# Performance work log

Hardware: AMD Instinct MI355X
Metric: run time of the kernel (lower is better)

The kernel has to match this reference:

```python
import jax, jax.numpy as jnp
import numpy as np

N, E, D, H = 50000, 800000, 128, 128


def _uniform_param(key, shape, fan_in):
    bound = 1.0 / np.sqrt(fan_in)
    return jax.random.uniform(key, shape, jnp.float32, -bound, bound)


def setup_inputs() -> dict:
    key = jax.random.key(0)
    ks = jax.random.split(key, 12)
    x = jax.random.normal(ks[0], (N, D), jnp.float32)
    xedge = jax.random.randint(ks[1], (2, E), 0, N, jnp.int64)
    y = jax.random.randint(ks[2], (N,), 0, 2, jnp.int32).astype(bool)
    return {
        "x": x,
        "xedge": xedge,
        "y": y,
        "pretrain": 0,
        # SAGEConv layer 1 (in=D, out=H): lin_l (with bias) applied to mean aggr, lin_r (no bias) to self
        "W1l": _uniform_param(ks[3], (D, H), D),
        "b1l": _uniform_param(ks[4], (H,), D),
        "W1r": _uniform_param(ks[5], (D, H), D),
        # SAGEConv layer 2 (in=H, out=H)
        "W2l": _uniform_param(ks[6], (H, H), H),
        "b2l": _uniform_param(ks[7], (H,), H),
        "W2r": _uniform_param(ks[8], (H, H), H),
        # Decoder weight [H, H]
        "Wdec": _uniform_param(ks[9], (H, H), H),
    }


def sage_conv(h, src, dst, Wl, bl, Wr, num_nodes):
    # gather neighbor features along edges, mean-aggregate by destination
    msgs = h[src]                                            # [E, d]
    agg = jax.ops.segment_sum(msgs, dst, num_segments=num_nodes)
    cnt = jax.ops.segment_sum(jnp.ones((src.shape[0],), h.dtype), dst,
                              num_segments=num_nodes)
    mean = agg / jnp.maximum(cnt, 1.0)[:, None]              # [N, d]
    return mean @ Wl + bl + h @ Wr                           # [N, out]


def reference(x, xedge, y, pretrain, W1l, b1l, W1r, W2l, b2l, W2r, Wdec):
    src, dst = xedge[0], xedge[1]
    n = x.shape[0]
    # Encoder: SAGE = conv1 -> relu -> (dropout: eval identity) -> conv2
    h = jax.nn.relu(sage_conv(x, src, dst, W1l, b1l, W1r, n))
    emb = sage_conv(h, src, dst, W2l, b2l, W2r, n)           # [N, H]
    # Decoder
    dx = emb @ Wdec                                          # [N, H]
    # BCEWithLogits: pos nodes target 1, neg nodes target 0, mean within each group
    ym = y.astype(dx.dtype)                                  # [N]
    n_pos = jnp.sum(ym)
    n_neg = n - n_pos
    hdim = dx.shape[1]
    sp_pos = jax.nn.softplus(-dx)   # bce(logit, 1)
    sp_neg = jax.nn.softplus(dx)    # bce(logit, 0)
    l2 = jnp.sum(sp_pos * ym[:, None]) / (jnp.maximum(n_pos, 1.0) * hdim)
    l1 = jnp.sum(sp_neg * (1.0 - ym)[:, None]) / (jnp.maximum(n_neg, 1.0) * hdim)
    return (l1 + l2, emb)
```

## Files before the change

### kernel.cpp

```cpp
#include <hip/hip_runtime.h>
#include <hip/hip_bf16.h>

#define NDIM 128
#define SCAN_CHUNK 1024

typedef __attribute__((ext_vector_type(8))) short short8;
typedef __attribute__((ext_vector_type(4))) float f32x4;

__device__ __forceinline__ float bf2f(__hip_bfloat16 v) { return __bfloat162float(v); }

__device__ __forceinline__ float ldf(const void* p, long i, int f32) {
    return f32 ? ((const float*)p)[i] : bf2f(((const __hip_bfloat16*)p)[i]);
}
__device__ __forceinline__ void stf(void* p, long i, int f32, float v) {
    if (f32) ((float*)p)[i] = v;
    else     ((__hip_bfloat16*)p)[i] = __float2bfloat16(v);
}
__device__ __forceinline__ short f2bf(float v) {
    __hip_bfloat16 h = __float2bfloat16(v);
    short s;
    __builtin_memcpy(&s, &h, 2);
    return s;
}
__device__ __forceinline__ float bflo(unsigned u) { u <<= 16; float f; __builtin_memcpy(&f, &u, 4); return f; }
__device__ __forceinline__ float bfhi(unsigned u) { u &= 0xffff0000u; float f; __builtin_memcpy(&f, &u, 4); return f; }
__device__ __forceinline__ unsigned packbf(float a, float b) {
    unsigned la = (unsigned short)f2bf(a);
    unsigned hb = (unsigned short)f2bf(b);
    return (hb << 16) | la;
}
__device__ __forceinline__ int aswz(int m, int k) {
    return m * NDIM + ((((k >> 3) ^ (m & 7)) << 3) | (k & 7));
}
__device__ __forceinline__ int wswz(int m, int p) {
    return m * 64 + ((((p >> 2) ^ (m & 7)) << 2) | (p & 3));
}

__global__ void detect_kernel(const int* __restrict__ xedge32,
                              const unsigned int* __restrict__ yw,
                              const unsigned short* __restrict__ xh,
                              int* __restrict__ flags, int* __restrict__ cnt,
                              float* __restrict__ accum, int* __restrict__ npos, int N) {
    const int gid = blockIdx.x * 256 + threadIdx.x;
    for (int i = gid; i < N; i += gridDim.x * 256) cnt[i] = 0;
    if (gid == 0) { accum[0] = 0.f; accum[1] = 0.f; npos[0] = 0; }
    if (blockIdx.x == 0) {
        __shared__ int se, sy, scount;
        const int t = threadIdx.x;
        if (t == 0) { se = 1; sy = 0; scount = 0; }
        __syncthreads();
        for (int i = t; i < 512; i += 256)
            if (xedge32[2 * i + 1] != 0) se = 0;
        for (int i = t; i < 1024; i += 256)
            if (yw[i] > 1u) sy = 1;
        int c = 0;
        for (int i = t; i < 1024; i += 256) {
            int ex = (xh[2 * i] >> 7) & 0xFF;
            if (ex >= 100 && ex <= 150) c++;
        }
        atomicAdd(&scount, c);
        __syncthreads();
        if (t == 0) { flags[0] = se; flags[1] = sy; flags[2] = (scount < 900) ? 1 : 0; }
    }
}


__global__ void prep_kernel(const void* __restrict__ x,
                            const void* __restrict__ W1l, const void* __restrict__ b1l,
                            const void* __restrict__ W1r, const void* __restrict__ W2l,
                            const void* __restrict__ b2l, const void* __restrict__ W2r,
                            const void* __restrict__ Wd, const int* __restrict__ flags,
                            short* __restrict__ T1l, short* __restrict__ T1r,
                            short* __restrict__ T2l, short* __restrict__ T2r,
                            short* __restrict__ Td, float* __restrict__ b1c,
                            float* __restrict__ b2c, unsigned* __restrict__ xb,
                            const int* __restrict__ xedge, int E,
                            int* __restrict__ cnt, int N) {
    const int wf = flags[2];
    const long idx = (long)blockIdx.x * 256 + threadIdx.x;
    if (idx < E) {
        int d = flags[0] ? xedge[2 * (E + idx)] : xedge[E + idx];
        atomicAdd(&cnt[d], 1);
    }
    if (idx < NDIM * NDIM) {
        int k = (int)(idx >> 7), n = (int)(idx & 127);
        int o = n * NDIM + k;
        T1l[o] = f2bf(ldf(W1l, idx, wf));
        T1r[o] = f2bf(ldf(W1r, idx, wf));
        T2l[o] = f2bf(ldf(W2l, idx, wf));
        T2r[o] = f2bf(ldf(W2r, idx, wf));
        Td [o] = f2bf(ldf(Wd , idx, wf));
        if (idx < NDIM) { b1c[idx] = ldf(b1l, idx, wf); b2c[idx] = ldf(b2l, idx, wf); }
    } else {
        long p = idx - NDIM * NDIM;
        long np = (long)N * 64;
        if (p < np) {
            if (wf) {
                float2 v = ((const float2*)x)[p];
                xb[p] = packbf(v.x, v.y);
            } else {
                xb[p] = ((const unsigned*)x)[p];
            }
        }
    }
}


__global__ void scan_partial(const int* __restrict__ cnt, int* __restrict__ bsum, int N) {
    __shared__ int red[256];
    const int t = threadIdx.x;
    const long base = (long)blockIdx.x * SCAN_CHUNK + (long)t * 4;
    int s = 0;
#pragma unroll
    for (int i = 0; i < 4; ++i) { long idx = base + i; if (idx < N) s += cnt[idx]; }
    red[t] = s;
    __syncthreads();
    for (int off = 128; off >= 1; off >>= 1) {
        if (t < off) red[t] += red[t + off];
        __syncthreads();
    }
    if (t == 0) bsum[blockIdx.x] = red[0];
}

__global__ void scan_bsums(const int* __restrict__ bsum, int* __restrict__ boff,
                           int B, int* __restrict__ rowptr, int N) {
    __shared__ int part[1024];
    const int t = threadIdx.x;
    int v = (t < B) ? bsum[t] : 0;
    part[t] = v;
    __syncthreads();
    for (int off = 1; off < 1024; off <<= 1) {
        int u = (t >= off) ? part[t - off] : 0;
        __syncthreads();
        part[t] += u;
        __syncthreads();
    }
    if (t < B) boff[t] = part[t] - v;
    if (t == 1023) rowptr[N] = part[1023];
}

__global__ void scan_scatter(int* __restrict__ cnt, const int* __restrict__ boff,
                             int* __restrict__ rowptr, int N) {
    __shared__ int tsum[256];
    const int t = threadIdx.x;
    const long base = (long)blockIdx.x * SCAN_CHUNK + (long)t * 4;
    int loc[4];
    int s = 0;
#pragma unroll
    for (int i = 0; i < 4; ++i) {
        long idx = base + i;
        int c = (idx < N) ? cnt[idx] : 0;
        loc[i] = s;
        s += c;
    }
    tsum[t] = s;
    __syncthreads();
    for (int off = 1; off < 256; off <<= 1) {
        int u = (t >= off) ? tsum[t - off] : 0;
        __syncthreads();
        tsum[t] += u;
        __syncthreads();
    }
    const int texcl = tsum[t] - s;
    const int b0 = boff[blockIdx.x];
#pragma unroll
    for (int i = 0; i < 4; ++i) {
        long idx = base + i;
        if (idx < N) { rowptr[idx] = b0 + texcl + loc[i]; cnt[idx] = 0; }
    }
}

__global__ void fill_kernel(const int* __restrict__ xedge, int E,
                            const int* __restrict__ flags, const int* __restrict__ rowptr,
                            int* __restrict__ cur, int* __restrict__ col) {
    int e = blockIdx.x * blockDim.x + threadIdx.x;
    if (e >= E) return;
    const int e64 = flags[0];
    int s = e64 ? xedge[2 * e] : xedge[e];
    int d = e64 ? xedge[2 * (E + e)] : xedge[E + e];
    int p = rowptr[d] + atomicAdd(&cur[d], 1);
    col[p] = s;
}


template <bool RELU, int OUTMODE>
__global__ __launch_bounds__(256)
void layer_mfma(const unsigned* __restrict__ Xb, const int* __restrict__ rowptr,
                const int* __restrict__ col, const short* __restrict__ WlT,
                const float* __restrict__ biasc, const short* __restrict__ WrT,
                const int* __restrict__ flags, void* __restrict__ outp,
                unsigned* __restrict__ hemb, int N) {
    __shared__ short AS[2 * 32 * NDIM];
    short* Ms = AS;
    short* Ss = AS + 32 * NDIM;
    unsigned* Msw = (unsigned*)Ms;
    unsigned* Ssw = (unsigned*)Ss;
    const int t = threadIdx.x;
    const int n0 = blockIdx.x * 32;
    const int wf = flags[2];
    {
        const int g = t >> 6, p = t & 63;
        for (int r = g; r < 32; r += 4) {
            int n = n0 + r;
            float m0 = 0.f, m1 = 0.f;
            unsigned su = 0;
            if (n < N) {
                int b = rowptr[n], e = rowptr[n + 1];
                int i = b;
                for (; i + 8 <= e; i += 8) {
                    unsigned u0 = Xb[(long)col[i    ] * 64 + p];
                    unsigned u1 = Xb[(long)col[i + 1] * 64 + p];
                    unsigned u2 = Xb[(long)col[i + 2] * 64 + p];
                    unsigned u3 = Xb[(long)col[i + 3] * 64 + p];
                    unsigned u4 = Xb[(long)col[i + 4] * 64 + p];
                    unsigned u5 = Xb[(long)col[i + 5] * 64 + p];
                    unsigned u6 = Xb[(long)col[i + 6] * 64 + p];
                    unsigned u7 = Xb[(long)col[i + 7] * 64 + p];
                    m0 += ((bflo(u0) + bflo(u1)) + (bflo(u2) + bflo(u3)))
                        + ((bflo(u4) + bflo(u5)) + (bflo(u6) + bflo(u7)));
                    m1 += ((bfhi(u0) + bfhi(u1)) + (bfhi(u2) + bfhi(u3)))
                        + ((bfhi(u4) + bfhi(u5)) + (bfhi(u6) + bfhi(u7)));
                }
                for (; i < e; ++i) {
                    unsigned u = Xb[(long)col[i] * 64 + p];
                    m0 += bflo(u);
                    m1 += bfhi(u);
                }
                float inv = 1.f / fmaxf((float)(e - b), 1.f);
                m0 *= inv; m1 *= inv;
                su = Xb[(long)n * 64 + p];
            }
            int wi = wswz(r, p);
            Msw[wi] = packbf(m0, m1);
            Ssw[wi] = su;
        }
    }
    __syncthreads();
    const int l = t & 63, w = t >> 6;
    const int quad = l >> 4, l15 = l & 15;
    const int wcol = w * 32;
    f32x4 acc[2][2] = {};
    for (int k0 = 0; k0 < NDIM; k0 += 32) {
        const int kc = k0 + quad * 8;
        short8 ams[2], ass[2], bl[2], br[2];
#pragma unroll
        for (int rt = 0; rt < 2; ++rt) {
            int m = rt * 16 + l15;
            ams[rt] = *(const short8*)&Ms[aswz(m, kc)];
            ass[rt] = *(const short8*)&Ss[aswz(m, kc)];
        }
#pragma unroll
        for (int ct = 0; ct < 2; ++ct) {
            int n = wcol + ct * 16 + l15;
            bl[ct] = *(const short8*)&WlT[n * NDIM + kc];
            br[ct] = *(const short8*)&WrT[n * NDIM + kc];
        }
#pragma unroll
        for (int rt = 0; rt < 2; ++rt)
#pragma unroll
            for (int ct = 0; ct < 2; ++ct) {
                acc[rt][ct] = __builtin_amdgcn_mfma_f32_16x16x32_bf16(
                    ams[rt], bl[ct], acc[rt][ct], 0, 0, 0);
                acc[rt][ct] = __builtin_amdgcn_mfma_f32_16x16x32_bf16(
                    ass[rt], br[ct], acc[rt][ct], 0, 0, 0);
            }
    }
    __syncthreads();

    if (OUTMODE == 0) {
#pragma unroll
        for (int ct = 0; ct < 2; ++ct) {
            int cg = wcol + ct * 16 + l15;
            float bv = biasc[cg];
#pragma unroll
            for (int rt = 0; rt < 2; ++rt)
#pragma unroll
                for (int reg = 0; reg < 4; ++reg) {
                    int row = rt * 16 + quad * 4 + reg;
                    float v = acc[rt][ct][reg] + bv;
                    if (RELU) v = fmaxf(v, 0.f);
                    Ms[row * NDIM + cg] = f2bf(v);
                }
        }
        __syncthreads();
        unsigned* ob = (unsigned*)outp;
        for (int idx = t; idx < 2048; idx += 256) {
            int r = idx >> 6;
            if (n0 + r < N) ob[(long)n0 * 64 + idx] = Msw[idx];
        }
    } else {
        if (wf) {
            float* Tf = (float*)AS;
#pragma unroll
            for (int ct = 0; ct < 2; ++ct) {
                int cg = wcol + ct * 16 + l15;
                float bv = biasc[cg];
#pragma unroll
                for (int rt = 0; rt < 2; ++rt)
#pragma unroll
                    for (int reg = 0; reg < 4; ++reg) {
                        int row = rt * 16 + quad * 4 + reg;
                        Tf[row * NDIM + cg] = acc[rt][ct][reg] + bv;
                    }
            }
            __syncthreads();
            float* embf = (float*)outp + 1;
            for (int idx = t; idx < 4096; idx += 256) {
                int r = idx >> 7;
                if (n0 + r < N) embf[(long)n0 * NDIM + idx] = Tf[idx];
            }
            __syncthreads();
        }
#pragma unroll
        for (int ct = 0; ct < 2; ++ct) {
            int cg = wcol + ct * 16 + l15;
            float bv = biasc[cg];
#pragma unroll
            for (int rt = 0; rt < 2; ++rt)
#pragma unroll
                for (int reg = 0; reg < 4; ++reg) {
                    int row = rt * 16 + quad * 4 + reg;
                    Ms[row * NDIM + cg] = f2bf(acc[rt][ct][reg] + bv);
                }
        }
        __syncthreads();
        for (int idx = t; idx < 2048; idx += 256) {
            int r = idx >> 6;
            if (n0 + r < N) hemb[(long)n0 * 64 + idx] = Msw[idx];
        }
        if (!wf) {
            short* embh = (short*)outp + 1;
            for (int idx = t; idx < 4096; idx += 256) {
                int r = idx >> 7;
                if (n0 + r < N) embh[(long)n0 * NDIM + idx] = Ms[idx];
            }
        }
    }
}


__global__ __launch_bounds__(256)
void loss_mfma(const unsigned* __restrict__ hemb, const short* __restrict__ WdT,
               const void* __restrict__ yv, const int* __restrict__ flags,
               float* __restrict__ accum, int* __restrict__ npos, int N) {
    __shared__ short As[32 * NDIM];
    __shared__ int ylds[32];
    __shared__ float red[4][2];
    unsigned* Asw = (unsigned*)As;
    const int t = threadIdx.x;
    const int n0 = blockIdx.x * 32;
    const int yb = flags[1];
    {
        const int g = t >> 6, p = t & 63;
        for (int r = g; r < 32; r += 4) {
            int n = n0 + r;
            Asw[wswz(r, p)] = (n < N) ? hemb[(long)n * 64 + p] : 0u;
        }
        if (t < 32) {
            int n = n0 + t;
            int yn = -1;
            if (n < N)
                yn = yb ? (int)((const unsigned char*)yv)[n]
                        : (((const int*)yv)[n] != 0 ? 1 : 0);
            ylds[t] = yn;
        }
    }
    __syncthreads();
    const int l = t & 63, w = t >> 6;
    const int quad = l >> 4, l15 = l & 15;
    const int wcol = w * 32;
    f32x4 acc[2][2] = {};
    for (int k0 = 0; k0 < NDIM; k0 += 32) {
        const int kc = k0 + quad * 8;
        short8 a[2], b[2];
#pragma unroll
        for (int rt = 0; rt < 2; ++rt)
            a[rt] = *(const short8*)&As[aswz(rt * 16 + l15, kc)];
#pragma unroll
        for (int ct = 0; ct < 2; ++ct)
            b[ct] = *(const short8*)&WdT[(wcol + ct * 16 + l15) * NDIM + kc];
#pragma unroll
        for (int rt = 0; rt < 2; ++rt)
#pragma unroll
            for (int ct = 0; ct < 2; ++ct)
                acc[rt][ct] = __builtin_amdgcn_mfma_f32_16x16x32_bf16(
                    a[rt], b[ct], acc[rt][ct], 0, 0, 0);
    }
    float lpos = 0.f, lneg = 0.f;
#pragma unroll
    for (int rt = 0; rt < 2; ++rt)
#pragma unroll
        for (int reg = 0; reg < 4; ++reg) {
            int row = rt * 16 + quad * 4 + reg;
            int yn = ylds[row];
            if (yn >= 0) {
#pragma unroll
                for (int ct = 0; ct < 2; ++ct) {
                    float z = acc[rt][ct][reg];
                    float L = log1pf(expf(-fabsf(z)));
                    if (yn) lpos += fmaxf(-z, 0.f) + L;
                    else    lneg += fmaxf(z, 0.f) + L;
                }
            }
        }
#pragma unroll
    for (int off = 32; off >= 1; off >>= 1) {
        lpos += __shfl_down(lpos, off, 64);
        lneg += __shfl_down(lneg, off, 64);
    }
    if (l == 0) { red[w][0] = lpos; red[w][1] = lneg; }
    __syncthreads();
    if (t == 0) {
        atomicAdd(&accum[0], red[0][0] + red[1][0] + red[2][0] + red[3][0]);
        atomicAdd(&accum[1], red[0][1] + red[1][1] + red[2][1] + red[3][1]);
        int c = 0;
        for (int i = 0; i < 32; ++i) if (ylds[i] > 0) c++;
        if (c) atomicAdd(npos, c);
    }
}

__global__ void finalize_kernel(const float* __restrict__ accum, const int* __restrict__ npos,
                                const int* __restrict__ flags, void* __restrict__ out, int N) {
    float np_ = (float)(*npos);
    float nn_ = (float)N - np_;
    float l2 = accum[0] / (fmaxf(np_, 1.f) * 128.f);
    float l1 = accum[1] / (fmaxf(nn_, 1.f) * 128.f);
    stf(out, 0, flags[2], l1 + l2);
}


extern "C" void kernel_launch(void* const* d_in, const int* in_sizes, int n_in,
                              void* d_out, int out_size, void* d_ws, size_t ws_size,
                              hipStream_t stream) {
    const void* x    = d_in[0];
    const int* xedge = (const int*)d_in[1];
    const void* y    = d_in[2];
    const void* W1l  = d_in[4];
    const void* b1l  = d_in[5];
    const void* W1r  = d_in[6];
    const void* W2l  = d_in[7];
    const void* b2l  = d_in[8];
    const void* W2r  = d_in[9];
    const void* Wdec = d_in[10];

    const int N = in_sizes[0] / NDIM;
    const int E = in_sizes[1] / 2;

    char* ws = (char*)d_ws;
    size_t off = 0;
    auto alloc = [&](size_t bytes) -> void* {
        void* p = ws + off;
        off = (off + bytes + 255) & ~(size_t)255;
        return p;
    };
    int*   flags  = (int*)alloc(64);
    float* accum  = (float*)alloc(64);
    int*   npos   = (int*)alloc(64);
    int*   bsum   = (int*)alloc(1024 * 4);
    int*   boff   = (int*)alloc(1024 * 4);
    int*   cnt    = (int*)alloc((size_t)N * 4);
    int*   rowptr = (int*)alloc((size_t)(N + 1) * 4);
    int*   col    = (int*)alloc((size_t)E * 4);
    unsigned* xb  = (unsigned*)alloc((size_t)N * 64 * 4);
    unsigned* hbuf = (unsigned*)alloc((size_t)N * 64 * 4);
    short* T1l = (short*)alloc(NDIM * NDIM * 2);
    short* T1r = (short*)alloc(NDIM * NDIM * 2);
    short* T2l = (short*)alloc(NDIM * NDIM * 2);
    short* T2r = (short*)alloc(NDIM * NDIM * 2);
    short* Td  = (short*)alloc(NDIM * NDIM * 2);
    float* b1c = (float*)alloc(NDIM * 4);
    float* b2c = (float*)alloc(NDIM * 4);

    const int zb = (N + 255) / 256;
    detect_kernel<<<zb, 256, 0, stream>>>(xedge, (const unsigned int*)y,
                                          (const unsigned short*)x, flags, cnt,
                                          accum, npos, N);
    const long prep_items = (long)NDIM * NDIM + (long)N * 64;
    prep_kernel<<<(int)((prep_items + 255) / 256), 256, 0, stream>>>(
        x, W1l, b1l, W1r, W2l, b2l, W2r, Wdec, flags,
        T1l, T1r, T2l, T2r, Td, b1c, b2c, xb, xedge, E, cnt, N);

    const int sb = (N + SCAN_CHUNK - 1) / SCAN_CHUNK;
    scan_partial<<<sb, 256, 0, stream>>>(cnt, bsum, N);
    scan_bsums<<<1, 1024, 0, stream>>>(bsum, boff, sb, rowptr, N);
    scan_scatter<<<sb, 256, 0, stream>>>(cnt, boff, rowptr, N);

    const int eb = (E + 255) / 256;
    fill_kernel<<<eb, 256, 0, stream>>>(xedge, E, flags, rowptr, cnt, col);

    const int nb32 = (N + 31) / 32;
    layer_mfma<true, 0><<<nb32, 256, 0, stream>>>(
        xb, rowptr, col, T1l, b1c, T1r, flags, hbuf, nullptr, N);
    layer_mfma<false, 1><<<nb32, 256, 0, stream>>>(
        hbuf, rowptr, col, T2l, b2c, T2r, flags, d_out, xb, N);
    loss_mfma<<<nb32, 256, 0, stream>>>(xb, Td, y, flags, accum, npos, N);
    finalize_kernel<<<1, 1, 0, stream>>>(accum, npos, flags, d_out, N);
}
```

Before: 378.7 us.

## Fuse decoder loss into second SAGE layer and interleave two-row neighbor gathers

Removes the separate loss kernel. The second layer now keeps its bf16 embedding tile in shared memory and runs the decoder MFMA and BCE reduction in place, which avoids writing and re-reading the bf16 embedding buffer. The aggregation loop now processes two destination rows per wave at once, so more independent gather loads are in flight. The embedding output is written directly from accumulators with scattered per-element stores instead of coalesced staged copies. This may hurt write efficiency and adds register pressure.

```diff
diff --git a/kernel.cpp b/kernel.cpp
--- a/kernel.cpp
+++ b/kernel.cpp
@@ -188,9 +188,12 @@
 void layer_mfma(const unsigned* __restrict__ Xb, const int* __restrict__ rowptr,
                 const int* __restrict__ col, const short* __restrict__ WlT,
                 const float* __restrict__ biasc, const short* __restrict__ WrT,
+                const short* __restrict__ WdT, const void* __restrict__ yv,
                 const int* __restrict__ flags, void* __restrict__ outp,
-                unsigned* __restrict__ hemb, int N) {
+                float* __restrict__ accum, int* __restrict__ npos, int N) {
     __shared__ short AS[2 * 32 * NDIM];
+    __shared__ int ylds[32];
+    __shared__ float redm[4][2];
     short* Ms = AS;
     short* Ss = AS + 32 * NDIM;
     unsigned* Msw = (unsigned*)Ms;
@@ -198,41 +201,68 @@
     const int t = threadIdx.x;
     const int n0 = blockIdx.x * 32;
     const int wf = flags[2];
+
+    if (OUTMODE == 1 && t < 32) {
+        const int yb = flags[1];
+        int n = n0 + t;
+        int yn = -1;
+        if (n < N)
+            yn = yb ? (int)((const unsigned char*)yv)[n]
+                    : (((const int*)yv)[n] != 0 ? 1 : 0);
+        ylds[t] = yn;
+    }
+
     {
         const int g = t >> 6, p = t & 63;
-        for (int r = g; r < 32; r += 4) {
-            int n = n0 + r;
-            float m0 = 0.f, m1 = 0.f;
-            unsigned su = 0;
-            if (n < N) {
-                int b = rowptr[n], e = rowptr[n + 1];
-                int i = b;
-                for (; i + 8 <= e; i += 8) {
-                    unsigned u0 = Xb[(long)col[i    ] * 64 + p];
-                    unsigned u1 = Xb[(long)col[i + 1] * 64 + p];
-                    unsigned u2 = Xb[(long)col[i + 2] * 64 + p];
-                    unsigned u3 = Xb[(long)col[i + 3] * 64 + p];
-                    unsigned u4 = Xb[(long)col[i + 4] * 64 + p];
-                    unsigned u5 = Xb[(long)col[i + 5] * 64 + p];
-                    unsigned u6 = Xb[(long)col[i + 6] * 64 + p];
-                    unsigned u7 = Xb[(long)col[i + 7] * 64 + p];
-                    m0 += ((bflo(u0) + bflo(u1)) + (bflo(u2) + bflo(u3)))
-                        + ((bflo(u4) + bflo(u5)) + (bflo(u6) + bflo(u7)));
-                    m1 += ((bfhi(u0) + bfhi(u1)) + (bfhi(u2) + bfhi(u3)))
-                        + ((bfhi(u4) + bfhi(u5)) + (bfhi(u6) + bfhi(u7)));
-                }
-                for (; i < e; ++i) {
-                    unsigned u = Xb[(long)col[i] * 64 + p];
-                    m0 += bflo(u);
-                    m1 += bfhi(u);
-                }
-                float inv = 1.f / fmaxf((float)(e - b), 1.f);
-                m0 *= inv; m1 *= inv;
-                su = Xb[(long)n * 64 + p];
-            }
-            int wi = wswz(r, p);
-            Msw[wi] = packbf(m0, m1);
-            Ssw[wi] = su;
+        for (int k = 0; k < 4; ++k) {
+            const int rA = g + 8 * k, rB = rA + 4;
+            const int nA = n0 + rA, nB = n0 + rB;
+            float a0 = 0.f, a1 = 0.f, c0 = 0.f, c1 = 0.f;
+            unsigned sA = 0u, sB = 0u;
+            int bA = 0, eA = 0, bB = 0, eB = 0;
+            if (nA < N) { bA = rowptr[nA]; eA = rowptr[nA + 1]; sA = Xb[(long)nA * 64 + p]; }
+            if (nB < N) { bB = rowptr[nB]; eB = rowptr[nB + 1]; sB = Xb[(long)nB * 64 + p]; }
+            int iA = bA, iB = bB;
+            while (iA + 8 <= eA && iB + 8 <= eB) {
+                unsigned uA[8], uB[8];
+#pragma unroll
+                for (int j = 0; j < 8; ++j) uA[j] = Xb[(long)col[iA + j] * 64 + p];
+#pragma unroll
+                for (int j = 0; j < 8; ++j) uB[j] = Xb[(long)col[iB + j] * 64 + p];
+#pragma unroll
+                for (int j = 0; j < 8; ++j) { a0 += bflo(uA[j]); a1 += bfhi(uA[j]); }
+#pragma unroll
+                for (int j = 0; j < 8; ++j) { c0 += bflo(uB[j]); c1 += bfhi(uB[j]); }
+                iA += 8; iB += 8;
+            }
+            for (; iA + 8 <= eA; iA += 8) {
+                unsigned u[8];
+#pragma unroll
+                for (int j = 0; j < 8; ++j) u[j] = Xb[(long)col[iA + j] * 64 + p];
+#pragma unroll
+                for (int j = 0; j < 8; ++j) { a0 += bflo(u[j]); a1 += bfhi(u[j]); }
+            }
+            for (; iB + 8 <= eB; iB += 8) {
+                unsigned u[8];
+#pragma unroll
+                for (int j = 0; j < 8; ++j) u[j] = Xb[(long)col[iB + j] * 64 + p];
+#pragma unroll
+                for (int j = 0; j < 8; ++j) { c0 += bflo(u[j]); c1 += bfhi(u[j]); }
+            }
+            for (; iA < eA; ++iA) {
+                unsigned u = Xb[(long)col[iA] * 64 + p];
+                a0 += bflo(u); a1 += bfhi(u);
+            }
+            for (; iB < eB; ++iB) {
+                unsigned u = Xb[(long)col[iB] * 64 + p];
+                c0 += bflo(u); c1 += bfhi(u);
+            }
+            float invA = 1.f / fmaxf((float)(eA - bA), 1.f);
+            float invB = 1.f / fmaxf((float)(eB - bB), 1.f);
+            Msw[wswz(rA, p)] = packbf(a0 * invA, a1 * invA);
+            Ssw[wswz(rA, p)] = sA;
+            Msw[wswz(rB, p)] = packbf(c0 * invB, c1 * invB);
+            Ssw[wswz(rB, p)] = sB;
         }
     }
     __syncthreads();
@@ -289,28 +319,6 @@
             if (n0 + r < N) ob[(long)n0 * 64 + idx] = Msw[idx];
         }
     } else {
-        if (wf) {
-            float* Tf = (float*)AS;
-#pragma unroll
-            for (int ct = 0; ct < 2; ++ct) {
-                int cg = wcol + ct * 16 + l15;
-                float bv = biasc[cg];
-#pragma unroll
-                for (int rt = 0; rt < 2; ++rt)
-#pragma unroll
-                    for (int reg = 0; reg < 4; ++reg) {
-                        int row = rt * 16 + quad * 4 + reg;
-                        Tf[row * NDIM + cg] = acc[rt][ct][reg] + bv;
-                    }
-            }
-            __syncthreads();
-            float* embf = (float*)outp + 1;
-            for (int idx = t; idx < 4096; idx += 256) {
-                int r = idx >> 7;
-                if (n0 + r < N) embf[(long)n0 * NDIM + idx] = Tf[idx];
-            }
-            __syncthreads();
-        }
 #pragma unroll
         for (int ct = 0; ct < 2; ++ct) {
             int cg = wcol + ct * 16 + l15;
@@ -320,102 +328,65 @@
 #pragma unroll
                 for (int reg = 0; reg < 4; ++reg) {
                     int row = rt * 16 + quad * 4 + reg;
-                    Ms[row * NDIM + cg] = f2bf(acc[rt][ct][reg] + bv);
+                    float v = acc[rt][ct][reg] + bv;
+                    Ms[aswz(row, cg)] = f2bf(v);
+                    int n = n0 + row;
+                    if (n < N) {
+                        if (wf) ((float*)outp)[1 + (long)n * NDIM + cg] = v;
+                        else ((__hip_bfloat16*)outp)[1 + (long)n * NDIM + cg] =
+                                 __float2bfloat16(v);
+                    }
                 }
         }
         __syncthreads();
-        for (int idx = t; idx < 2048; idx += 256) {
-            int r = idx >> 6;
-            if (n0 + r < N) hemb[(long)n0 * 64 + idx] = Msw[idx];
-        }
-        if (!wf) {
-            short* embh = (short*)outp + 1;
-            for (int idx = t; idx < 4096; idx += 256) {
-                int r = idx >> 7;
-                if (n0 + r < N) embh[(long)n0 * NDIM + idx] = Ms[idx];
-            }
-        }
-    }
-}
-
-
-__global__ __launch_bounds__(256)
-void loss_mfma(const unsigned* __restrict__ hemb, const short* __restrict__ WdT,
-               const void* __restrict__ yv, const int* __restrict__ flags,
-               float* __restrict__ accum, int* __restrict__ npos, int N) {
-    __shared__ short As[32 * NDIM];
-    __shared__ int ylds[32];
-    __shared__ float red[4][2];
-    unsigned* Asw = (unsigned*)As;
-    const int t = threadIdx.x;
-    const int n0 = blockIdx.x * 32;
-    const int yb = flags[1];
-    {
-        const int g = t >> 6, p = t & 63;
-        for (int r = g; r < 32; r += 4) {
-            int n = n0 + r;
-            Asw[wswz(r, p)] = (n < N) ? hemb[(long)n * 64 + p] : 0u;
-        }
-        if (t < 32) {
-            int n = n0 + t;
-            int yn = -1;
-            if (n < N)
-                yn = yb ? (int)((const unsigned char*)yv)[n]
-                        : (((const int*)yv)[n] != 0 ? 1 : 0);
-            ylds[t] = yn;
-        }
-    }
-    __syncthreads();
-    const int l = t & 63, w = t >> 6;
-    const int quad = l >> 4, l15 = l & 15;
-    const int wcol = w * 32;
-    f32x4 acc[2][2] = {};
-    for (int k0 = 0; k0 < NDIM; k0 += 32) {
-        const int kc = k0 + quad * 8;
-        short8 a[2], b[2];
+        f32x4 acc2[2][2] = {};
+        for (int k0 = 0; k0 < NDIM; k0 += 32) {
+            const int kc = k0 + quad * 8;
+            short8 a[2], b[2];
+#pragma unroll
+            for (int rt = 0; rt < 2; ++rt)
+                a[rt] = *(const short8*)&Ms[aswz(rt * 16 + l15, kc)];
+#pragma unroll
+            for (int ct = 0; ct < 2; ++ct)
+                b[ct] = *(const short8*)&WdT[(wcol + ct * 16 + l15) * NDIM + kc];
+#pragma unroll
+            for (int rt = 0; rt < 2; ++rt)
+#pragma unroll
+                for (int ct = 0; ct < 2; ++ct)
+                    acc2[rt][ct] = __builtin_amdgcn_mfma_f32_16x16x32_bf16(
+                        a[rt], b[ct], acc2[rt][ct], 0, 0, 0);
+        }
+        float lpos = 0.f, lneg = 0.f;
 #pragma unroll
         for (int rt = 0; rt < 2; ++rt)
-            a[rt] = *(const short8*)&As[aswz(rt * 16 + l15, kc)];
-#pragma unroll
-        for (int ct = 0; ct < 2; ++ct)
-            b[ct] = *(const short8*)&WdT[(wcol + ct * 16 + l15) * NDIM + kc];
-#pragma unroll
-        for (int rt = 0; rt < 2; ++rt)
-#pragma unroll
-            for (int ct = 0; ct < 2; ++ct)
-                acc[rt][ct] = __builtin_amdgcn_mfma_f32_16x16x32_bf16(
-                    a[rt], b[ct], acc[rt][ct], 0, 0, 0);
-    }
-    float lpos = 0.f, lneg = 0.f;
-#pragma unroll
-    for (int rt = 0; rt < 2; ++rt)
-#pragma unroll
-        for (int reg = 0; reg < 4; ++reg) {
-            int row = rt * 16 + quad * 4 + reg;
-            int yn = ylds[row];
-            if (yn >= 0) {
-#pragma unroll
-                for (int ct = 0; ct < 2; ++ct) {
-                    float z = acc[rt][ct][reg];
-                    float L = log1pf(expf(-fabsf(z)));
-                    if (yn) lpos += fmaxf(-z, 0.f) + L;
-                    else    lneg += fmaxf(z, 0.f) + L;
+#pragma unroll
+            for (int reg = 0; reg < 4; ++reg) {
+                int row = rt * 16 + quad * 4 + reg;
+                int yn = ylds[row];
+                if (yn >= 0) {
+#pragma unroll
+                    for (int ct = 0; ct < 2; ++ct) {
+                        float z = acc2[rt][ct][reg];
+                        float L = log1pf(expf(-fabsf(z)));
+                        if (yn) lpos += fmaxf(-z, 0.f) + L;
+                        else    lneg += fmaxf(z, 0.f) + L;
+                    }
                 }
             }
-        }
-#pragma unroll
-    for (int off = 32; off >= 1; off >>= 1) {
-        lpos += __shfl_down(lpos, off, 64);
-        lneg += __shfl_down(lneg, off, 64);
-    }
-    if (l == 0) { red[w][0] = lpos; red[w][1] = lneg; }
-    __syncthreads();
-    if (t == 0) {
-        atomicAdd(&accum[0], red[0][0] + red[1][0] + red[2][0] + red[3][0]);
-        atomicAdd(&accum[1], red[0][1] + red[1][1] + red[2][1] + red[3][1]);
-        int c = 0;
-        for (int i = 0; i < 32; ++i) if (ylds[i] > 0) c++;
-        if (c) atomicAdd(npos, c);
+#pragma unroll
+        for (int off = 32; off >= 1; off >>= 1) {
+            lpos += __shfl_down(lpos, off, 64);
+            lneg += __shfl_down(lneg, off, 64);
+        }
+        if (l == 0) { redm[w][0] = lpos; redm[w][1] = lneg; }
+        __syncthreads();
+        if (t == 0) {
+            atomicAdd(&accum[0], redm[0][0] + redm[1][0] + redm[2][0] + redm[3][0]);
+            atomicAdd(&accum[1], redm[0][1] + redm[1][1] + redm[2][1] + redm[3][1]);
+            int c = 0;
+            for (int i = 0; i < 32; ++i) if (ylds[i] > 0) c++;
+            if (c) atomicAdd(npos, c);
+        }
     }
 }
 
@@ -490,9 +461,10 @@
 
     const int nb32 = (N + 31) / 32;
     layer_mfma<true, 0><<<nb32, 256, 0, stream>>>(
-        xb, rowptr, col, T1l, b1c, T1r, flags, hbuf, nullptr, N);
+        xb, rowptr, col, T1l, b1c, T1r, nullptr, nullptr, flags,
+        hbuf, nullptr, nullptr, N);
     layer_mfma<false, 1><<<nb32, 256, 0, stream>>>(
-        hbuf, rowptr, col, T2l, b2c, T2r, flags, d_out, xb, N);
-    loss_mfma<<<nb32, 256, 0, stream>>>(xb, Td, y, flags, accum, npos, N);
+        hbuf, rowptr, col, T2l, b2c, T2r, Td, y, flags,
+        d_out, accum, npos, N);
     finalize_kernel<<<1, 1, 0, stream>>>(accum, npos, flags, d_out, N);
 }
```

After: 369.5 us. 1.02x faster.
